# Performance work log

Hardware: AMD Instinct MI355X
Metric: run time of the kernel (lower is better)

## Reference

```python
import jax, jax.numpy as jnp
import numpy as np

# ---- configuration matching init_kwargs ----
WINDOW = (0, 20000)
WIDTH = float(WINDOW[1] - WINDOW[0])
NBINS = (32, 64, 128)   # number of bins per binset; boundaries have nbins-1 entries
HIDDEN = 32
N_GENES = 512
N_FRAG = 2_000_000
N_MOTIF = 5_000_000


def _make_bins(nb):
    # interior boundaries of nb equal-width bins over [0, WIDTH)
    return jnp.asarray(np.linspace(0.0, WIDTH, nb + 1)[1:-1], dtype=jnp.float32)


def setup_inputs() -> dict:
    key = jax.random.key(0)
    ks = jax.random.split(key, 8)
    coordinates = jax.random.randint(ks[0], (N_FRAG,), 0, WINDOW[1], dtype=jnp.int32)
    frag_local_gene_ix = jax.random.randint(ks[1], (N_FRAG,), 0, N_GENES, dtype=jnp.int32)
    motif_positions = jax.random.randint(ks[2], (N_MOTIF,), 0, WINDOW[1], dtype=jnp.int32)
    motif_local_gene_ix = jax.random.randint(ks[3], (N_MOTIF,), 0, N_GENES, dtype=jnp.int32)
    # per-binset predictor MLP params (same shapes for every binset -> stacked)
    K = len(NBINS)
    W1 = jax.random.normal(ks[4], (K, 1, HIDDEN), dtype=jnp.float32) * 0.1
    B1 = jnp.zeros((K, HIDDEN), dtype=jnp.float32)
    W2 = jax.random.normal(ks[5], (K, HIDDEN, 1), dtype=jnp.float32) * 0.1
    B2 = jnp.zeros((K, 1), dtype=jnp.float32)
    return {
        "coordinates": coordinates,
        "frag_local_gene_ix": frag_local_gene_ix,
        "motif_positions": motif_positions,
        "motif_local_gene_ix": motif_local_gene_ix,
        "bins0": _make_bins(NBINS[0]),
        "bins1": _make_bins(NBINS[1]),
        "bins2": _make_bins(NBINS[2]),
        "W1": W1, "B1": B1, "W2": W2, "B2": B2,
    }


def reference(coordinates, frag_local_gene_ix, motif_positions,
              motif_local_gene_ix, bins0, bins1, bins2, W1, B1, W2, B2):
    coords_f = coordinates.astype(jnp.float32)          # window[0] == 0 -> already shifted
    mot_pos_f = motif_positions.astype(jnp.float32)
    lp = jnp.zeros((coordinates.shape[0],), dtype=jnp.float32)
    ones = jnp.ones((motif_positions.shape[0],), dtype=jnp.float32)
    for k, bins in enumerate((bins0, bins1, bins2)):
        nb = bins.shape[0] + 1                          # len(binset)+1 bins
        bw = bins[1] - bins[0]
        # histogram of motif hits per (gene, bin): searchsorted + bincount
        idx_m = jnp.searchsorted(bins, mot_pos_f)
        seg = motif_local_gene_ix * nb + idx_m          # local_gene_ix * (len+1) + bin
        counts = jax.ops.segment_sum(ones, seg, num_segments=N_GENES * nb) / bw
        # per-bin MLP predictor: 1 -> HIDDEN -> 1 on bincount
        h = jax.nn.relu(counts[:, None] @ W1[k] + B1[k]) @ W2[k] + B2[k]  # [G*nb, 1]
        heights = h.reshape(N_GENES, nb)                # unnormalized heights per gene
        logits = jax.nn.log_softmax(heights, axis=-1)
        # piecewise-constant density log_prob for each fragment coordinate
        idx_c = jnp.searchsorted(bins, coords_f)
        lp = lp + logits[frag_local_gene_ix, idx_c] + jnp.log(jnp.float32(nb))
    return lp - jnp.log(jnp.float32(WIDTH))
```

## Files before the change

kernel.cpp:

```cpp
#include <hip/hip_runtime.h>
#include <hip/hip_bf16.h>
#include <hip/hip_fp16.h>
#include <math.h>

#define NGENES 512
#define NB2 128
#define HIST_ELEMS (NGENES * NB2)
#define NBLK 256
#define IMG_WORDS (HIST_ELEMS / 8)
#define UNROLL 4
#define T_BYTES (HIST_ELEMS * 2)

typedef int   v4i __attribute__((ext_vector_type(4)));
typedef unsigned int v4u __attribute__((ext_vector_type(4)));
typedef float v4f __attribute__((ext_vector_type(4)));

__device__ __forceinline__ int fine_idx(int v) {
    int i = (4 * v - 1) / 625;
    i = i < 0 ? 0 : i;
    return i > 127 ? 127 : i;
}

__global__ __launch_bounds__(1024) void hist_u4_kernel(const int* __restrict__ pos,
                                                       const int* __restrict__ gene,
                                                       unsigned int* __restrict__ partial,
                                                       int nm, int chunk) {
    __shared__ unsigned int lds[IMG_WORDS];
    const int p = blockIdx.x;

    v4u* lds4 = (v4u*)lds;
    for (int i = threadIdx.x; i < IMG_WORDS / 4; i += 1024) {
        v4u z = {0u, 0u, 0u, 0u};
        lds4[i] = z;
    }
    __syncthreads();

    const int start = p * chunk;
    const int end   = min(start + chunk, nm);
    const int i4s = start >> 2;
    const int i4e = end >> 2;
    const v4i* p4 = (const v4i*)pos;
    const v4i* g4 = (const v4i*)gene;

    int base = i4s;
    for (; base + UNROLL * 1024 <= i4e; base += UNROLL * 1024) {
        v4i P[UNROLL], G[UNROLL];
#pragma unroll
        for (int k = 0; k < UNROLL; ++k) {
            const int i = base + k * 1024 + (int)threadIdx.x;
            P[k] = p4[i];
            G[k] = g4[i];
        }
#pragma unroll
        for (int k = 0; k < UNROLL; ++k) {
            int c0 = (G[k].x << 7) + fine_idx(P[k].x);
            int c1 = (G[k].y << 7) + fine_idx(P[k].y);
            int c2 = (G[k].z << 7) + fine_idx(P[k].z);
            int c3 = (G[k].w << 7) + fine_idx(P[k].w);
            atomicAdd(&lds[c0 >> 3], 1u << ((c0 & 7) << 2));
            atomicAdd(&lds[c1 >> 3], 1u << ((c1 & 7) << 2));
            atomicAdd(&lds[c2 >> 3], 1u << ((c2 & 7) << 2));
            atomicAdd(&lds[c3 >> 3], 1u << ((c3 & 7) << 2));
        }
    }
    for (int i = base + (int)threadIdx.x; i < i4e; i += 1024) {
        v4i pp = p4[i];
        v4i gg = g4[i];
        int c0 = (gg.x << 7) + fine_idx(pp.x);
        int c1 = (gg.y << 7) + fine_idx(pp.y);
        int c2 = (gg.z << 7) + fine_idx(pp.z);
        int c3 = (gg.w << 7) + fine_idx(pp.w);
        atomicAdd(&lds[c0 >> 3], 1u << ((c0 & 7) << 2));
        atomicAdd(&lds[c1 >> 3], 1u << ((c1 & 7) << 2));
        atomicAdd(&lds[c2 >> 3], 1u << ((c2 & 7) << 2));
        atomicAdd(&lds[c3 >> 3], 1u << ((c3 & 7) << 2));
    }
    for (int i = i4e * 4 + (int)threadIdx.x; i < end; i += 1024) {
        int c = (gene[i] << 7) + fine_idx(pos[i]);
        atomicAdd(&lds[c >> 3], 1u << ((c & 7) << 2));
    }
    __syncthreads();

    v4u* dst = (v4u*)(partial + (size_t)p * IMG_WORDS);
    for (int i = threadIdx.x; i < IMG_WORDS / 4; i += 1024) dst[i] = lds4[i];
}

__global__ void hist_kernel(const int* __restrict__ pos, const int* __restrict__ gene,
                            unsigned int* __restrict__ hist, int n) {
    const int tid = blockIdx.x * blockDim.x + threadIdx.x;
    const int stride = gridDim.x * blockDim.x;
    const int n4 = n >> 2;
    const v4i* p4 = (const v4i*)pos;
    const v4i* g4 = (const v4i*)gene;
    for (int i = tid; i < n4; i += stride) {
        v4i p = p4[i];
        v4i g = g4[i];
        atomicAdd(&hist[(g.x << 7) + fine_idx(p.x)], 1u);
        atomicAdd(&hist[(g.y << 7) + fine_idx(p.y)], 1u);
        atomicAdd(&hist[(g.z << 7) + fine_idx(p.z)], 1u);
        atomicAdd(&hist[(g.w << 7) + fine_idx(p.w)], 1u);
    }
    int t = n4 * 4 + tid;
    if (t < n) atomicAdd(&hist[(gene[t] << 7) + fine_idx(pos[t])], 1u);
}

__device__ __forceinline__ float mlp32(float c, const float* __restrict__ W1k,
                                       const float* __restrict__ B1k,
                                       const float* __restrict__ W2k, float b2) {
    float s = b2;
#pragma unroll
    for (int h = 0; h < 32; ++h) {
        float v = fmaf(c, W1k[h], B1k[h]);
        v = v > 0.f ? v : 0.f;
        s = fmaf(v, W2k[h], s);
    }
    return s;
}

__device__ __forceinline__ float wave_max(float v) {
#pragma unroll
    for (int off = 32; off >= 1; off >>= 1) v = fmaxf(v, __shfl_xor(v, off));
    return v;
}
__device__ __forceinline__ float wave_sum(float v) {
#pragma unroll
    for (int off = 32; off >= 1; off >>= 1) v += __shfl_xor(v, off);
    return v;
}

__device__ __forceinline__ void table_math(int g, int t, float n2a, float n2b,
                                           const float* __restrict__ W1,
                                           const float* __restrict__ B1,
                                           const float* __restrict__ W2,
                                           const float* __restrict__ B2,
                                           __half* __restrict__ T) {
    float n1 = n2a + n2b;
    float n0 = __shfl(n1, 2 * t) + __shfl(n1, 2 * t + 1);

    float h2a = mlp32(n2a / 156.25f, W1 + 64, B1 + 64, W2 + 64, B2[2]);
    float h2b = mlp32(n2b / 156.25f, W1 + 64, B1 + 64, W2 + 64, B2[2]);
    float h1  = mlp32(n1  / 312.5f,  W1 + 32, B1 + 32, W2 + 32, B2[1]);
    float h0  = mlp32(n0  / 625.0f,  W1,      B1,      W2,      B2[0]);

    float m2 = wave_max(fmaxf(h2a, h2b));
    float s2 = wave_sum(expf(h2a - m2) + expf(h2b - m2));
    float l2 = m2 + logf(s2);

    float m1 = wave_max(h1);
    float s1 = wave_sum(expf(h1 - m1));
    float l1 = m1 + logf(s1);

    float h0m = (t < 32) ? h0 : -INFINITY;
    float m0 = wave_max(h0m);
    float s0 = wave_sum((t < 32) ? expf(h0 - m0) : 0.f);
    float l0 = m0 + logf(s0);

    const float CONST = logf(32.f) + logf(64.f) + logf(128.f) - logf(20000.f);

    float ls1 = h1 - l1;
    float ls0_own = h0 - l0;
    float ls0 = __shfl(ls0_own, t >> 1);

    float base = ls1 + ls0 + CONST;
    T[(g << 7) + 2 * t]     = __float2half((h2a - l2) + base);
    T[(g << 7) + 2 * t + 1] = __float2half((h2b - l2) + base);
}

__global__ __launch_bounds__(512) void table_from_partial(const unsigned int* __restrict__ partial,
                                                          const float* __restrict__ W1,
                                                          const float* __restrict__ B1,
                                                          const float* __restrict__ W2,
                                                          const float* __restrict__ B2,
                                                          __half* __restrict__ T) {
    const int g = blockIdx.x;
    const int t = threadIdx.x & 63;
    const int w = threadIdx.x >> 6;
    __shared__ unsigned int sa[8][64];
    __shared__ unsigned int sb[8][64];

    const unsigned char* src = (const unsigned char*)partial + (g << 6) + t;
    unsigned int n2a = 0, n2b = 0;
#pragma unroll 8
    for (int p = w * (NBLK / 8); p < (w + 1) * (NBLK / 8); ++p) {
        unsigned char v = src[(size_t)p * (IMG_WORDS * 4)];
        n2a += v & 0xFu;
        n2b += v >> 4;
    }
    sa[w][t] = n2a;
    sb[w][t] = n2b;
    __syncthreads();

    if (threadIdx.x < 64) {
        unsigned int fa = 0, fb = 0;
#pragma unroll
        for (int k = 0; k < 8; ++k) { fa += sa[k][t]; fb += sb[k][t]; }
        table_math(g, t, (float)fa, (float)fb, W1, B1, W2, B2, T);
    }
}

__global__ __launch_bounds__(64) void table_from_hist(const unsigned int* __restrict__ hist,
                                                      const float* __restrict__ W1,
                                                      const float* __restrict__ B1,
                                                      const float* __restrict__ W2,
                                                      const float* __restrict__ B2,
                                                      __half* __restrict__ T) {
    const int g = blockIdx.x;
    const int t = threadIdx.x;
    const unsigned int* hg = hist + (g << 7);
    table_math(g, t, (float)hg[2 * t], (float)hg[2 * t + 1], W1, B1, W2, B2, T);
}

__global__ __launch_bounds__(1024) void gather_lds_kernel(const int* __restrict__ coord,
                                                          const int* __restrict__ gene,
                                                          const __half* __restrict__ Th,
                                                          float* __restrict__ out, int n) {
    extern __shared__ __half Tl[];
    {
        const v4u* src = (const v4u*)Th;
        v4u* dst = (v4u*)Tl;
#pragma unroll
        for (int k = 0; k < T_BYTES / 16 / 1024; ++k)
            dst[k * 1024 + threadIdx.x] = src[k * 1024 + threadIdx.x];
    }
    __syncthreads();

    const int tid = blockIdx.x * 1024 + (int)threadIdx.x;
    const int stride = NBLK * 1024;
    const int n8 = n >> 3;
    const v4i* c4 = (const v4i*)coord;
    const v4i* g4 = (const v4i*)gene;
    v4f* o4 = (v4f*)out;
    for (int i = tid; i < n8; i += stride) {
        v4i c0 = c4[2 * i];
        v4i c1 = c4[2 * i + 1];
        v4i g0 = g4[2 * i];
        v4i g1 = g4[2 * i + 1];
        v4f oa, ob;
        oa.x = __half2float(Tl[(g0.x << 7) + fine_idx(c0.x)]);
        oa.y = __half2float(Tl[(g0.y << 7) + fine_idx(c0.y)]);
        oa.z = __half2float(Tl[(g0.z << 7) + fine_idx(c0.z)]);
        oa.w = __half2float(Tl[(g0.w << 7) + fine_idx(c0.w)]);
        ob.x = __half2float(Tl[(g1.x << 7) + fine_idx(c1.x)]);
        ob.y = __half2float(Tl[(g1.y << 7) + fine_idx(c1.y)]);
        ob.z = __half2float(Tl[(g1.z << 7) + fine_idx(c1.z)]);
        ob.w = __half2float(Tl[(g1.w << 7) + fine_idx(c1.w)]);
        o4[2 * i]     = oa;
        o4[2 * i + 1] = ob;
    }
    for (int t = n8 * 8 + tid; t < n; t += stride)
        out[t] = __half2float(Tl[(gene[t] << 7) + fine_idx(coord[t])]);
}

__global__ __launch_bounds__(256) void frag_kernel(const int* __restrict__ coord,
                                                   const int* __restrict__ gene,
                                                   const __half* __restrict__ T,
                                                   float* __restrict__ out, int n) {
    const int tid = blockIdx.x * blockDim.x + threadIdx.x;
    const int stride = gridDim.x * blockDim.x;
    const int n4 = n >> 2;
    const v4i* c4 = (const v4i*)coord;
    const v4i* g4 = (const v4i*)gene;
    v4f* o4 = (v4f*)out;
    for (int i = tid; i < n4; i += stride) {
        v4i c = c4[i];
        v4i g = g4[i];
        v4f o;
        o.x = __half2float(T[(g.x << 7) + fine_idx(c.x)]);
        o.y = __half2float(T[(g.y << 7) + fine_idx(c.y)]);
        o.z = __half2float(T[(g.z << 7) + fine_idx(c.z)]);
        o.w = __half2float(T[(g.w << 7) + fine_idx(c.w)]);
        o4[i] = o;
    }
    for (int t = n4 * 4 + tid; t < n; t += stride)
        out[t] = __half2float(T[(gene[t] << 7) + fine_idx(coord[t])]);
}

extern "C" void kernel_launch(void* const* d_in, const int* in_sizes, int n_in,
                              void* d_out, int out_size, void* d_ws, size_t ws_size,
                              hipStream_t stream) {
    const int* coords = (const int*)d_in[0];
    const int* fgene  = (const int*)d_in[1];
    const int* mpos   = (const int*)d_in[2];
    const int* mgene  = (const int*)d_in[3];
    const float* W1 = (const float*)d_in[7];
    const float* B1 = (const float*)d_in[8];
    const float* W2 = (const float*)d_in[9];
    const float* B2 = (const float*)d_in[10];

    __half* Th = (__half*)d_ws;
    unsigned int* hist = (unsigned int*)((char*)d_ws + T_BYTES);
    unsigned int* partial = (unsigned int*)((char*)d_ws + T_BYTES
                                            + HIST_ELEMS * sizeof(unsigned int));

    const int nf = in_sizes[0];
    const int nm = in_sizes[2];

    const size_t need = T_BYTES + HIST_ELEMS * sizeof(unsigned int)
                      + (size_t)NBLK * IMG_WORDS * sizeof(unsigned int);

    if (ws_size >= need) {
        int chunk = ((nm + NBLK - 1) / NBLK + 3) & ~3;
        hist_u4_kernel<<<NBLK, 1024, 0, stream>>>(mpos, mgene, partial, nm, chunk);
        table_from_partial<<<NGENES, 512, 0, stream>>>(partial, W1, B1, W2, B2, Th);
        gather_lds_kernel<<<NBLK, 1024, T_BYTES, stream>>>(coords, fgene, Th, (float*)d_out, nf);
    } else {
        (void)hipMemsetAsync(hist, 0, HIST_ELEMS * sizeof(unsigned int), stream);
        hist_kernel<<<2048, 256, 0, stream>>>(mpos, mgene, hist, nm);
        table_from_hist<<<NGENES, 64, 0, stream>>>(hist, W1, B1, W2, B2, Th);
        frag_kernel<<<1024, 256, 0, stream>>>(coords, fgene, Th, (float*)d_out, nf);
    }
}
```

Baseline: 28.53 us.

## Interleave per-block partial histograms by gene for coalesced vector reduction

The histogram kernel now writes its per-block nibble-packed partial histograms interleaved so that each gene's data from all 256 blocks sits in one contiguous 16 KB region. The table kernel then reads that region with coalesced 16-byte loads and does SWAR byte-lane accumulation, instead of strided single-byte loads spread across 256 separate images. It merges results through LDS atomics into 16-bit packed bin pairs. This trades scattered writes in the histogram kernel and 8-bit lane overflow limits for much better read coalescing in the reduction.

```diff
diff --git a/kernel.cpp b/kernel.cpp
--- a/kernel.cpp
+++ b/kernel.cpp
@@ -81,8 +81,9 @@
     }
     __syncthreads();
 
-    v4u* dst = (v4u*)(partial + (size_t)p * IMG_WORDS);
-    for (int i = threadIdx.x; i < IMG_WORDS / 4; i += 1024) dst[i] = lds4[i];
+    v4u* dst = (v4u*)partial;
+    for (int j = threadIdx.x; j < IMG_WORDS / 4; j += 1024)
+        dst[((j >> 2) << 10) + (p << 2) + (j & 3)] = lds4[j];
 }
 
 __global__ void hist_kernel(const int* __restrict__ pos, const int* __restrict__ gene,
@@ -166,36 +167,46 @@
     T[(g << 7) + 2 * t + 1] = __float2half((h2b - l2) + base);
 }
 
-__global__ __launch_bounds__(512) void table_from_partial(const unsigned int* __restrict__ partial,
+__global__ __launch_bounds__(256) void table_from_partial(const unsigned int* __restrict__ partial,
                                                           const float* __restrict__ W1,
                                                           const float* __restrict__ B1,
                                                           const float* __restrict__ W2,
                                                           const float* __restrict__ B2,
                                                           __half* __restrict__ T) {
     const int g = blockIdx.x;
-    const int t = threadIdx.x & 63;
-    const int w = threadIdx.x >> 6;
-    __shared__ unsigned int sa[8][64];
-    __shared__ unsigned int sb[8][64];
-
-    const unsigned char* src = (const unsigned char*)partial + (g << 6) + t;
-    unsigned int n2a = 0, n2b = 0;
-#pragma unroll 8
-    for (int p = w * (NBLK / 8); p < (w + 1) * (NBLK / 8); ++p) {
-        unsigned char v = src[(size_t)p * (IMG_WORDS * 4)];
-        n2a += v & 0xFu;
-        n2b += v >> 4;
-    }
-    sa[w][t] = n2a;
-    sb[w][t] = n2b;
-    __syncthreads();
-
-    if (threadIdx.x < 64) {
-        unsigned int fa = 0, fb = 0;
-#pragma unroll
-        for (int k = 0; k < 8; ++k) { fa += sa[k][t]; fb += sb[k][t]; }
-        table_math(g, t, (float)fa, (float)fb, W1, B1, W2, B2, T);
-    }
+    const int t = threadIdx.x;
+    __shared__ unsigned int binpair[64];
+    if (t < 64) binpair[t] = 0u;
+    __syncthreads();
+
+    const v4u* src = (const v4u*)partial + (size_t)g * 1024;
+    unsigned int ae[4] = {0u, 0u, 0u, 0u};
+    unsigned int ao[4] = {0u, 0u, 0u, 0u};
+#pragma unroll
+    for (int r = 0; r < 4; ++r) {
+        v4u v = src[t + r * 256];
+#pragma unroll
+        for (int m = 0; m < 4; ++m) {
+            unsigned int w = v[m];
+            ae[m] += w & 0x0F0F0F0Fu;
+            ao[m] += (w >> 4) & 0x0F0F0F0Fu;
+        }
+    }
+    const int sub = t & 3;
+#pragma unroll
+    for (int m = 0; m < 4; ++m) {
+#pragma unroll
+        for (int k = 0; k < 4; ++k) {
+            unsigned int val = ((ae[m] >> (8 * k)) & 0xFFu)
+                             | (((ao[m] >> (8 * k)) & 0xFFu) << 16);
+            if (val) atomicAdd(&binpair[sub * 16 + m * 4 + k], val);
+        }
+    }
+    __syncthreads();
+
+    if (t < 64)
+        table_math(g, t, (float)(binpair[t] & 0xFFFFu), (float)(binpair[t] >> 16),
+                   W1, B1, W2, B2, T);
 }
 
 __global__ __launch_bounds__(64) void table_from_hist(const unsigned int* __restrict__ hist,
@@ -301,7 +312,7 @@
     if (ws_size >= need) {
         int chunk = ((nm + NBLK - 1) / NBLK + 3) & ~3;
         hist_u4_kernel<<<NBLK, 1024, 0, stream>>>(mpos, mgene, partial, nm, chunk);
-        table_from_partial<<<NGENES, 512, 0, stream>>>(partial, W1, B1, W2, B2, Th);
+        table_from_partial<<<NGENES, 256, 0, stream>>>(partial, W1, B1, W2, B2, Th);
         gather_lds_kernel<<<NBLK, 1024, T_BYTES, stream>>>(coords, fgene, Th, (float*)d_out, nf);
     } else {
         (void)hipMemsetAsync(hist, 0, HIST_ELEMS * sizeof(unsigned int), stream);
```

Measured after the change: 28.81 us. No clear change (+1.0%).
